# Kernel optimization log

Hardware: AMD Instinct MI355X
Metric: run time of the kernel (lower is better)

Reference implementation:

```python
import jax, jax.numpy as jnp
import numpy as np

DEPTH = 10
N_FEATURES = 1024
N_INTERNAL = 2 ** DEPTH - 1  # 1023
N_LEAVES = 2 ** DEPTH        # 1024
BATCH = 16384


def setup_inputs() -> dict:
    key = jax.random.key(0)
    k_x, k_w, k_b, k_leaf = jax.random.split(key, 4)
    x = jax.random.normal(k_x, (BATCH, N_FEATURES), dtype=jnp.float32)
    # stacked nn.Linear(n_features, 1) weights for all internal nodes
    bound = 1.0 / np.sqrt(N_FEATURES)
    W = jax.random.uniform(k_w, (N_INTERNAL, N_FEATURES), dtype=jnp.float32, minval=-bound, maxval=bound)
    b = jax.random.uniform(k_b, (N_INTERNAL,), dtype=jnp.float32, minval=-bound, maxval=bound)
    leaf_values = jax.random.normal(k_leaf, (N_LEAVES, 1), dtype=jnp.float32) * 0.01
    return {"x": x, "W": W, "b": b, "leaf_values": leaf_values}


def reference(x, W, b, leaf_values):
    # all node gates in one GEMM: [B, n_internal]
    gates = jax.nn.sigmoid(x @ W.T + b)
    # leaf path bits, MSB-first (matches path[::-1] in the original).
    # NOTE: original code increments node_index 0..depth-1 for every leaf
    # (it does NOT do binary-tree child indexing) -- replicated faithfully.
    leaf_ids = jnp.arange(N_LEAVES)
    shifts = DEPTH - 1 - jnp.arange(DEPTH)
    bits = ((leaf_ids[:, None] >> shifts[None, :]) & 1).astype(bool)  # [L, D]
    prob = jnp.ones((x.shape[0], N_LEAVES), dtype=x.dtype)  # [B, L]
    for d in range(DEPTH):  # small fixed loop over tree depth
        p = gates[:, d:d + 1]  # [B, 1]
        prob = prob * jnp.where(bits[:, d][None, :], p, 1.0 - p)
    return prob @ leaf_values  # [B, 1]
```

## Files before the change

kernel.cpp:

```cpp
#include <hip/hip_runtime.h>

#define BATCH   16384
#define NF      1024
#define NWAVES  4096
#define NROWS   (BATCH / NWAVES)


template <int CTRL>
__device__ __forceinline__ float dpp_add(float x) {
    int xi = __builtin_bit_cast(int, x);
    int yi = __builtin_amdgcn_update_dpp(xi, xi, CTRL, 0xf, 0xf, false);
    return x + __builtin_bit_cast(float, yi);
}

__device__ __forceinline__ float row_reduce_dpp(float x) {
    x = dpp_add<0xB1>(x);
    x = dpp_add<0x4E>(x);
    x = dpp_add<0x124>(x);
    x = dpp_add<0x128>(x);
    return x;
}

__device__ __forceinline__ float wave_sum(float x) {
    float r = row_reduce_dpp(x);
    int ri = __builtin_bit_cast(int, r);
    float s0 = __builtin_bit_cast(float, __builtin_amdgcn_readlane(ri, 0));
    float s1 = __builtin_bit_cast(float, __builtin_amdgcn_readlane(ri, 16));
    float s2 = __builtin_bit_cast(float, __builtin_amdgcn_readlane(ri, 32));
    float s3 = __builtin_bit_cast(float, __builtin_amdgcn_readlane(ri, 48));
    return (s0 + s1) + (s2 + s3);
}

__global__ __launch_bounds__(256, 2)
void sdt_kernel(const float* __restrict__ x,
                const float* __restrict__ W,
                const float* __restrict__ b,
                const float* __restrict__ leaf,
                float* __restrict__ out)
{
    const int lane = threadIdx.x & 63;
    const int wid  = (int)((blockIdx.x * blockDim.x + threadIdx.x) >> 6);

    __shared__ float lv_t[1024];
    {
        const int t = threadIdx.x * 4;
#pragma unroll
        for (int e = 0; e < 4; ++e) {
            int idx = t + e;
            lv_t[idx] = leaf[(idx & 63) * 16 + (idx >> 6)];
        }
    }

    float4 Wr[10][4];
#pragma unroll
    for (int d = 0; d < 10; ++d)
#pragma unroll
        for (int k = 0; k < 4; ++k)
            Wr[d][k] = *reinterpret_cast<const float4*>(W + d * NF + k * 256 + 4 * lane);

    float bias[10];
#pragma unroll
    for (int d = 0; d < 10; ++d) bias[d] = b[d];

    __syncthreads();

    auto load_row = [&](float4 (&dst)[4], int r) {
        const float* xr = x + (size_t)r * NF;
#pragma unroll
        for (int k = 0; k < 4; ++k)
            dst[k] = *reinterpret_cast<const float4*>(xr + k * 256 + 4 * lane);
    };

    auto process_row = [&](const float4 (&xv)[4], int row) {
        float acc[10];
#pragma unroll
        for (int d = 0; d < 10; ++d) {
            float a = 0.0f;
#pragma unroll
            for (int k = 0; k < 4; ++k) {
                a = fmaf(xv[k].x, Wr[d][k].x, a);
                a = fmaf(xv[k].y, Wr[d][k].y, a);
                a = fmaf(xv[k].z, Wr[d][k].z, a);
                a = fmaf(xv[k].w, Wr[d][k].w, a);
            }
            acc[d] = a;
        }
        float g[10];
#pragma unroll
        for (int d = 0; d < 10; ++d) {
            float z = wave_sum(acc[d]) + bias[d];
            g[d] = __builtin_amdgcn_rcpf(1.0f + __expf(-z));
        }
        float s9[8];
#pragma unroll
        for (int j = 0; j < 8; ++j) {
            float La = lv_t[(2 * j) * 64 + lane];
            float Lb = lv_t[(2 * j + 1) * 64 + lane];
            s9[j] = fmaf(g[9], Lb - La, La);
        }
        float s8[4];
#pragma unroll
        for (int j = 0; j < 4; ++j)
            s8[j] = fmaf(g[8], s9[2 * j + 1] - s9[2 * j], s9[2 * j]);
        float s7[2];
#pragma unroll
        for (int j = 0; j < 2; ++j)
            s7[j] = fmaf(g[7], s8[2 * j + 1] - s8[2 * j], s8[2 * j]);
        float s6 = fmaf(g[6], s7[1] - s7[0], s7[0]);

        float w = 1.0f;
#pragma unroll
        for (int d = 0; d < 6; ++d) {
            int bit = (lane >> (5 - d)) & 1;
            w *= bit ? g[d] : (1.0f - g[d]);
        }

        float v = wave_sum(w * s6);
        if (lane == 0) out[row] = v;
    };

    float4 xb0[4], xb1[4], xb2[4];
    load_row(xb0, wid);
    load_row(xb1, wid + 1 * NWAVES);

    load_row(xb2, wid + 2 * NWAVES); process_row(xb0, wid);
    load_row(xb0, wid + 3 * NWAVES); process_row(xb1, wid + 1 * NWAVES);
    process_row(xb2, wid + 2 * NWAVES);
    process_row(xb0, wid + 3 * NWAVES);
}

extern "C" void kernel_launch(void* const* d_in, const int* in_sizes, int n_in,
                              void* d_out, int out_size, void* d_ws, size_t ws_size,
                              hipStream_t stream) {
    const float* x    = (const float*)d_in[0];
    const float* W    = (const float*)d_in[1];
    const float* b    = (const float*)d_in[2];
    const float* leaf = (const float*)d_in[3];
    float* out = (float*)d_out;

    const int blocks  = 1024;
    const int threads = 256;

    sdt_kernel<<<blocks, threads, 0, stream>>>(x, W, b, leaf, out);
}
```

Baseline: 26.27 us.

## Split tree kernel into logits pass and separate leaf-combine pass

Splits the fused kernel in two. The first kernel streams x with half as many waves and a deeper 8-row load pipeline, and writes per-16-lane partial logits (with a quarter of the bias added) to workspace. The second kernel sums the partials, applies the sigmoid gates and does the leaf blend. This moves the cross-row reduction and leaf shared-memory setup out of the bandwidth-bound loop, at the cost of a second launch and an extra round trip through global memory. An empty asm barrier pins W in registers.

```diff
diff --git a/kernel.cpp b/kernel.cpp
--- a/kernel.cpp
+++ b/kernel.cpp
@@ -1,9 +1,9 @@
 #include <hip/hip_runtime.h>
 
-#define BATCH   16384
-#define NF      1024
-#define NWAVES  4096
-#define NROWS   (BATCH / NWAVES)
+#define BATCH    16384
+#define NF       1024
+#define NWAVES1  2048
+#define NWAVES2  4096
 
 
 template <int CTRL>
@@ -13,7 +13,7 @@
     return x + __builtin_bit_cast(float, yi);
 }
 
-__device__ __forceinline__ float row_reduce_dpp(float x) {
+__device__ __forceinline__ float group16_reduce(float x) {
     x = dpp_add<0xB1>(x);
     x = dpp_add<0x4E>(x);
     x = dpp_add<0x124>(x);
@@ -22,7 +22,7 @@
 }
 
 __device__ __forceinline__ float wave_sum(float x) {
-    float r = row_reduce_dpp(x);
+    float r = group16_reduce(x);
     int ri = __builtin_bit_cast(int, r);
     float s0 = __builtin_bit_cast(float, __builtin_amdgcn_readlane(ri, 0));
     float s1 = __builtin_bit_cast(float, __builtin_amdgcn_readlane(ri, 16));
@@ -32,24 +32,13 @@
 }
 
 __global__ __launch_bounds__(256, 2)
-void sdt_kernel(const float* __restrict__ x,
+void sdt_logits(const float* __restrict__ x,
                 const float* __restrict__ W,
                 const float* __restrict__ b,
-                const float* __restrict__ leaf,
-                float* __restrict__ out)
+                float* __restrict__ part)
 {
     const int lane = threadIdx.x & 63;
     const int wid  = (int)((blockIdx.x * blockDim.x + threadIdx.x) >> 6);
-
-    __shared__ float lv_t[1024];
-    {
-        const int t = threadIdx.x * 4;
-#pragma unroll
-        for (int e = 0; e < 4; ++e) {
-            int idx = t + e;
-            lv_t[idx] = leaf[(idx & 63) * 16 + (idx >> 6)];
-        }
-    }
 
     float4 Wr[10][4];
 #pragma unroll
@@ -57,12 +46,16 @@
 #pragma unroll
         for (int k = 0; k < 4; ++k)
             Wr[d][k] = *reinterpret_cast<const float4*>(W + d * NF + k * 256 + 4 * lane);
+#pragma unroll
+    for (int d = 0; d < 10; ++d)
+#pragma unroll
+        for (int k = 0; k < 4; ++k)
+            asm volatile("" : "+v"(Wr[d][k].x), "+v"(Wr[d][k].y),
+                              "+v"(Wr[d][k].z), "+v"(Wr[d][k].w));
 
-    float bias[10];
+    float bq[10];
 #pragma unroll
-    for (int d = 0; d < 10; ++d) bias[d] = b[d];
-
-    __syncthreads();
+    for (int d = 0; d < 10; ++d) bq[d] = b[d] * 0.25f;
 
     auto load_row = [&](float4 (&dst)[4], int r) {
         const float* xr = x + (size_t)r * NF;
@@ -85,12 +78,59 @@
             }
             acc[d] = a;
         }
+        float* pr = part + (size_t)row * 40 + (lane >> 4);
+        const bool st = (lane & 15) == 0;
+#pragma unroll
+        for (int d = 0; d < 10; ++d) {
+            float r = group16_reduce(acc[d]) + bq[d];
+            if (st) pr[d * 4] = r;
+        }
+    };
+
+    float4 xb0[4], xb1[4], xb2[4];
+    load_row(xb0, wid);
+    load_row(xb1, wid + 1 * NWAVES1);
+
+    load_row(xb2, wid + 2 * NWAVES1); process_row(xb0, wid);
+    load_row(xb0, wid + 3 * NWAVES1); process_row(xb1, wid + 1 * NWAVES1);
+    load_row(xb1, wid + 4 * NWAVES1); process_row(xb2, wid + 2 * NWAVES1);
+    load_row(xb2, wid + 5 * NWAVES1); process_row(xb0, wid + 3 * NWAVES1);
+    load_row(xb0, wid + 6 * NWAVES1); process_row(xb1, wid + 4 * NWAVES1);
+    load_row(xb1, wid + 7 * NWAVES1); process_row(xb2, wid + 5 * NWAVES1);
+    process_row(xb0, wid + 6 * NWAVES1);
+    process_row(xb1, wid + 7 * NWAVES1);
+}
+
+__global__ __launch_bounds__(256, 2)
+void sdt_combine(const float* __restrict__ part,
+                 const float* __restrict__ leaf,
+                 float* __restrict__ out)
+{
+    const int lane = threadIdx.x & 63;
+    const int wid  = (int)((blockIdx.x * blockDim.x + threadIdx.x) >> 6);
+
+    __shared__ float lv_t[1024];
+#pragma unroll
+    for (int e = 0; e < 4; ++e) {
+        int idx = threadIdx.x * 4 + e;
+        lv_t[idx] = leaf[(idx & 63) * 16 + (idx >> 6)];
+    }
+    __syncthreads();
+
+    for (int row = wid; row < BATCH; row += NWAVES2) {
+        float p = 0.0f;
+        if (lane < 40) p = part[(size_t)row * 40 + lane];
+        p = dpp_add<0xB1>(p);
+        p = dpp_add<0x4E>(p);
+
+        int pi = __builtin_bit_cast(int, p);
         float g[10];
 #pragma unroll
         for (int d = 0; d < 10; ++d) {
-            float z = wave_sum(acc[d]) + bias[d];
+            float z = __builtin_bit_cast(float, __builtin_amdgcn_readlane(pi, 4 * d));
             g[d] = __builtin_amdgcn_rcpf(1.0f + __expf(-z));
         }
+
         float s9[8];
 #pragma unroll
         for (int j = 0; j < 8; ++j) {
@@ -117,16 +157,7 @@
 
         float v = wave_sum(w * s6);
         if (lane == 0) out[row] = v;
-    };
-
-    float4 xb0[4], xb1[4], xb2[4];
-    load_row(xb0, wid);
-    load_row(xb1, wid + 1 * NWAVES);
-
-    load_row(xb2, wid + 2 * NWAVES); process_row(xb0, wid);
-    load_row(xb0, wid + 3 * NWAVES); process_row(xb1, wid + 1 * NWAVES);
-    process_row(xb2, wid + 2 * NWAVES);
-    process_row(xb0, wid + 3 * NWAVES);
+    }
 }
 
 extern "C" void kernel_launch(void* const* d_in, const int* in_sizes, int n_in,
@@ -136,10 +167,9 @@
     const float* W    = (const float*)d_in[1];
     const float* b    = (const float*)d_in[2];
     const float* leaf = (const float*)d_in[3];
-    float* out = (float*)d_out;
+    float* out  = (float*)d_out;
+    float* part = (float*)d_ws;
 
-    const int blocks  = 1024;
-    const int threads = 256;
-
-    sdt_kernel<<<blocks, threads, 0, stream>>>(x, W, b, leaf, out);
+    sdt_logits<<<512, 256, 0, stream>>>(x, W, b, part);
+    sdt_combine<<<1024, 256, 0, stream>>>(part, leaf, out);
 }
```

New measurement: 28.59 us. +8.9%, slower.
